# Optimization experiments

Hardware: AMD Instinct MI355X
Metric: run time of the kernel (lower is better)

## Reference

```python
import jax, jax.numpy as jnp
import numpy as np

NX, NA, T = 128, 64, 1024
MU = 1.0          # self.mu at entry to backward_pass
EPS = 1e-8        # singular-value clamp (self.eps)


def setup_inputs() -> dict:
    key = jax.random.key(0)
    ks = jax.random.split(key, 7)
    sx = 0.3 / np.sqrt(NX)  # keep dynamics spectral norm < 1 so recursion is stable
    fx = jax.random.normal(ks[0], (T, NX, NX), dtype=jnp.float32) * sx
    fa = jax.random.normal(ks[1], (T, NX, NA), dtype=jnp.float32) * sx
    lx = jax.random.normal(ks[2], (T, NX), dtype=jnp.float32)
    la = jax.random.normal(ks[3], (T, NA), dtype=jnp.float32)
    A = jax.random.normal(ks[4], (T, NX, NX), dtype=jnp.float32) * 0.1
    lxx = 0.5 * (A + A.transpose(0, 2, 1)) + jnp.eye(NX, dtype=jnp.float32)
    B = jax.random.normal(ks[5], (T, NA, NA), dtype=jnp.float32) * 0.1
    laa = 0.5 * (B + B.transpose(0, 2, 1)) + jnp.eye(NA, dtype=jnp.float32)
    lax = jax.random.normal(ks[6], (T, NA, NX), dtype=jnp.float32) * 0.1
    return dict(fx=fx, fa=fa, lx=lx, la=la, lxx=lxx, laa=laa, lax=lax)


def reference(fx, fa, lx, la, lxx, laa, lax):
    """iLQR backward Riccati recursion (ILQR.backward_pass + ILQR.q).
    Returns gains [T, na, 1+nx]: column 0 is k (feedforward), columns 1: are K
    (feedback), ordered by ascending time t=0..T-1."""
    I = jnp.eye(NX, dtype=fx.dtype)

    def step(carry, inp):
        Vx, Vxx = carry
        fx_t, fa_t, lx_t, la_t, lxx_t, laa_t, lax_t = inp
        # Q-function expansion (ILQR.q)
        Qx = lx_t + fx_t.T @ Vx
        Qa = la_t + fa_t.T @ Vx
        Qxx = lxx_t + fx_t.T @ Vxx @ fx_t
        Vreg = Vxx + MU * I
        Qax = lax_t + fa_t.T @ Vreg @ fx_t
        Qaa = laa_t + fa_t.T @ Vreg @ fa_t
        # SVD-based regularized inverse (S[S<eps] = eps)
        U, S, Vh = jnp.linalg.svd(Qaa)
        S = jnp.maximum(S, EPS)
        Vm = Vh.T
        Qaa_inv = (Vm * (1.0 / S)) @ U.T   # V diag(1/S) U^T
        Qaa_r = (U * S) @ Vm.T             # U diag(S) V^T (reconstructed Qaa)
        k = -Qaa_inv @ Qa
        K = -Qaa_inv @ Qax
        # value-function recursion
        Vx_n = Qx + K.T @ (Qaa_r @ k) + K.T @ Qa + Qax.T @ k
        Vxx_n = Qxx + K.T @ Qaa_r @ K + K.T @ Qax + Qax.T @ K
        Vxx_n = 0.5 * (Vxx_n + Vxx_n.T)
        return (Vx_n, Vxx_n), jnp.concatenate([k[:, None], K], axis=1)

    init = (lx[-1], lxx[-1])  # terminal Vx, Vxx
    (_, _), gains = jax.lax.scan(step, init, (fx, fa, lx, la, lxx, laa, lax), reverse=True)
    return gains
```

## Files before the change

kernel.cpp:

```cpp
#include <hip/hip_runtime.h>
#include <math.h>

#define TSTEPS 1024
#define NXD 128
#define NAD 64
#define NBLK 64
#define LSTR 67
#define QSTR 65
#define KSTR 68
#define GAINW 129

__device__ __forceinline__ float rdl(float v, int l) {
  return __int_as_float(__builtin_amdgcn_readlane(__float_as_int(v), l));
}
__device__ __forceinline__ double rdl(double v, int l) {
  unsigned long long b = (unsigned long long)__double_as_longlong(v);
  int lo = __builtin_amdgcn_readlane((int)(b & 0xffffffffULL), l);
  int hi = __builtin_amdgcn_readlane((int)(b >> 32), l);
  unsigned long long r = (((unsigned long long)(unsigned)hi) << 32) | (unsigned)lo;
  return __longlong_as_double((long long)r);
}

__device__ __forceinline__ float factor32(const float* __restrict__ QaaS, int lane,
                                          float* __restrict__ Lsh) {
  float a[64];
#pragma unroll
  for (int k = 0; k < 64; ++k) a[k] = QaaS[lane * QSTR + k];
  float mmax = 0.f;
#pragma unroll
  for (int j = 0; j < 63; ++j) {
    float d = rdl(a[j], j);
    d = (d == 0.f) ? 1e-30f : d;
    float rdv = 1.0f / d;
    float m = a[j] * rdv;
    m = (lane > j) ? m : 0.f;
    mmax = fmaxf(mmax, fabsf(m));
#pragma unroll
    for (int k = j + 1; k < 64; ++k) {
      float u = rdl(a[j], k);
      a[k] = fmaf(-m, u, a[k]);
    }
    if (lane > j) a[j] = m;
  }
#pragma unroll
  for (int k = 0; k < 64; ++k) Lsh[lane * LSTR + k] = a[k];
#pragma unroll
  for (int s = 1; s < 64; s <<= 1) mmax = fmaxf(mmax, __shfl_xor(mmax, s));
  return mmax;
}

__device__ __forceinline__ void factor64(const float* __restrict__ QaaS, int lane,
                                         double* __restrict__ Lsh) {
  double a[64];
#pragma unroll
  for (int k = 0; k < 64; ++k) a[k] = (double)QaaS[lane * QSTR + k];
#pragma unroll
  for (int j = 0; j < 63; ++j) {
    double d = rdl(a[j], j);
    d = (d == 0.0) ? 1e-300 : d;
    double rdv = 1.0 / d;
    double m = a[j] * rdv;
    m = (lane > j) ? m : 0.0;
#pragma unroll
    for (int k = j + 1; k < 64; ++k) {
      double u = rdl(a[j], k);
      a[k] = fma(-m, u, a[k]);
    }
    if (lane > j) a[j] = m;
  }
#pragma unroll
  for (int k = 0; k < 64; ++k) Lsh[lane * LSTR + k] = a[k];
}

template <typename T>
__device__ __forceinline__ void trisolveN(const T* __restrict__ Lsh, int lane,
                                          const float bv[9], float g[9]) {
  T x[9];
#pragma unroll
  for (int r = 0; r < 9; ++r) x[r] = (T)bv[r];
  for (int j = 0; j < 63; ++j) {
    T lij = Lsh[lane * LSTR + j];
#pragma unroll
    for (int r = 0; r < 9; ++r) {
      T xj = rdl(x[r], j);
      if (lane > j) x[r] = x[r] - lij * xj;
    }
  }
  T d = Lsh[lane * LSTR + lane];
  if (d == (T)0) d = (T)1e-30;
#pragma unroll
  for (int r = 0; r < 9; ++r) x[r] = x[r] / d;
  for (int j = 63; j > 0; --j) {
    T lji = Lsh[j * LSTR + lane];
#pragma unroll
    for (int r = 0; r < 9; ++r) {
      T xj = rdl(x[r], j);
      if (lane < j) x[r] = x[r] - lji * xj;
    }
  }
#pragma unroll
  for (int r = 0; r < 9; ++r) g[r] = -(float)x[r];
}

__device__ __forceinline__ void matvec128_lds(const float* __restrict__ VxxS, float fcl, float fch,
                                              int lane, float& w0, float& w1) {
  w0 = 0.f; w1 = 0.f;
  const float* vrow = VxxS + 2 * lane;
#pragma unroll 8
  for (int c = 0; c < 64; ++c) {
    float s = rdl(fcl, c);
    float2 v = *(const float2*)(vrow + c * NXD);
    w0 = fmaf(v.x, s, w0); w1 = fmaf(v.y, s, w1);
  }
#pragma unroll 8
  for (int c = 0; c < 64; ++c) {
    float s = rdl(fch, c);
    float2 v = *(const float2*)(vrow + (64 + c) * NXD);
    w0 = fmaf(v.x, s, w0); w1 = fmaf(v.y, s, w1);
  }
}

__global__ __launch_bounds__(256, 1) void k_init(const float* __restrict__ lxx,
                                                 const float* __restrict__ lx,
                                                 float* __restrict__ wsf) {
  float* Vxx = wsf;
  float* Vx  = wsf + 16384;
  const float* src = lxx + (size_t)(TSTEPS - 1) * NXD * NXD;
  int idx = blockIdx.x * 256 + threadIdx.x;
  Vxx[idx] = src[idx];
  if (blockIdx.x == 0 && threadIdx.x < NXD) Vx[threadIdx.x] = lx[(size_t)(TSTEPS - 1) * NXD + threadIdx.x];
}

__global__ __launch_bounds__(256, 1) void k_assemble(
    const float* __restrict__ fx, const float* __restrict__ fa,
    const float* __restrict__ lx, const float* __restrict__ la,
    const float* __restrict__ lxx, const float* __restrict__ laa,
    const float* __restrict__ lax, float* __restrict__ wsf, int t) {

  __shared__ float VxxS[NXD * NXD];

  const int b = blockIdx.x;
  const int tid = threadIdx.x;
  const int wave = tid >> 6;
  const int lane = tid & 63;

  float* Vxx  = wsf;
  float* Vx   = Vxx + 16384;
  float* QxxC = Vx + 128;
  float* QaxT = QxxC + 16384;
  float* QaaC = QaxT + 8192;
  float* Qx   = QaaC + 4096;
  float* Qa   = Qx + 128;

  const float* fxt  = fx  + (size_t)t * NXD * NXD;
  const float* fat  = fa  + (size_t)t * NXD * NAD;
  const float* lxt  = lx  + (size_t)t * NXD;
  const float* lat  = la  + (size_t)t * NAD;
  const float* lxxt = lxx + (size_t)t * NXD * NXD;
  const float* laat = laa + (size_t)t * NAD * NAD;
  const float* laxt = lax + (size_t)t * NAD * NXD;

  {
    const float4* Vg4 = (const float4*)Vxx;
    float4* Vs4 = (float4*)VxxS;
#pragma unroll
    for (int q = 0; q < 16; ++q) Vs4[tid + 256 * q] = Vg4[tid + 256 * q];
  }
  __syncthreads();

  if (wave <= 1) {
    const int j = 2 * b + wave;
    float pf0 = fxt[lane * NXD + j];
    float pf1 = fxt[(64 + lane) * NXD + j];
    float w0, w1;
    matvec128_lds(VxxS, pf0, pf1, lane, w0, w1);
    float q0 = lxxt[(size_t)(2 * lane) * NXD + j];
    float q1 = lxxt[(size_t)(2 * lane + 1) * NXD + j];
    float qa = laxt[lane * NXD + j];
#pragma unroll 4
    for (int r2 = 0; r2 < 32; ++r2) {
      float s0 = rdl(w0, r2), s1 = rdl(w1, r2);
      float t0 = s0 + rdl(pf0, 2 * r2);
      float t1 = s1 + rdl(pf0, 2 * r2 + 1);
      float2 f0 = *(const float2*)(fxt + (size_t)(2 * r2) * NXD + 2 * lane);
      float2 f1 = *(const float2*)(fxt + (size_t)(2 * r2 + 1) * NXD + 2 * lane);
      float g0 = fat[(2 * r2) * NAD + lane];
      float g1 = fat[(2 * r2 + 1) * NAD + lane];
      q0 = fmaf(f0.x, s0, q0); q1 = fmaf(f0.y, s0, q1);
      q0 = fmaf(f1.x, s1, q0); q1 = fmaf(f1.y, s1, q1);
      qa = fmaf(g0, t0, qa);   qa = fmaf(g1, t1, qa);
    }
#pragma unroll 4
    for (int r2 = 32; r2 < 64; ++r2) {
      float s0 = rdl(w0, r2), s1 = rdl(w1, r2);
      float t0 = s0 + rdl(pf1, 2 * r2 - 64);
      float t1 = s1 + rdl(pf1, 2 * r2 + 1 - 64);
      float2 f0 = *(const float2*)(fxt + (size_t)(2 * r2) * NXD + 2 * lane);
      float2 f1 = *(const float2*)(fxt + (size_t)(2 * r2 + 1) * NXD + 2 * lane);
      float g0 = fat[(2 * r2) * NAD + lane];
      float g1 = fat[(2 * r2 + 1) * NAD + lane];
      q0 = fmaf(f0.x, s0, q0); q1 = fmaf(f0.y, s0, q1);
      q0 = fmaf(f1.x, s1, q0); q1 = fmaf(f1.y, s1, q1);
      qa = fmaf(g0, t0, qa);   qa = fmaf(g1, t1, qa);
    }
    QxxC[(size_t)j * NXD + 2 * lane] = q0;
    QxxC[(size_t)j * NXD + 2 * lane + 1] = q1;
    QaxT[j * NAD + lane] = qa;
  } else if (wave == 2) {
    const int j = b;
    float pf0 = fat[lane * NAD + j];
    float pf1 = fat[(64 + lane) * NAD + j];
    float w0, w1;
    matvec128_lds(VxxS, pf0, pf1, lane, w0, w1);
    float qa = laat[lane * NAD + j];
#pragma unroll 4
    for (int r2 = 0; r2 < 32; ++r2) {
      float t0 = rdl(w0, r2) + rdl(pf0, 2 * r2);
      float t1 = rdl(w1, r2) + rdl(pf0, 2 * r2 + 1);
      float g0 = fat[(2 * r2) * NAD + lane];
      float g1 = fat[(2 * r2 + 1) * NAD + lane];
      qa = fmaf(g0, t0, qa); qa = fmaf(g1, t1, qa);
    }
#pragma unroll 4
    for (int r2 = 32; r2 < 64; ++r2) {
      float t0 = rdl(w0, r2) + rdl(pf1, 2 * r2 - 64);
      float t1 = rdl(w1, r2) + rdl(pf1, 2 * r2 + 1 - 64);
      float g0 = fat[(2 * r2) * NAD + lane];
      float g1 = fat[(2 * r2 + 1) * NAD + lane];
      qa = fmaf(g0, t0, qa); qa = fmaf(g1, t1, qa);
    }
    QaaC[j * NAD + lane] = qa;
  } else {
    float pv0 = Vx[lane], pv1 = Vx[64 + lane];
#pragma unroll
    for (int q = 0; q < 3; ++q) {
      int rr = 3 * b + q;
      float f0, f1;
      if (rr < NXD) { f0 = fxt[lane * NXD + rr]; f1 = fxt[(64 + lane) * NXD + rr]; }
      else { int aa = rr - NXD; f0 = fat[lane * NAD + aa]; f1 = fat[(64 + lane) * NAD + aa]; }
      float p = f0 * pv0 + f1 * pv1;
#pragma unroll
      for (int s = 1; s < 64; s <<= 1) p += __shfl_xor(p, s);
      if (lane == 0) {
        if (rr < NXD) Qx[rr] = lxt[rr] + p;
        else          Qa[rr - NXD] = lat[rr - NXD] + p;
      }
    }
  }
}

__global__ __launch_bounds__(256, 1) void k_solve_update(
    float* __restrict__ out, float* __restrict__ wsf, int t) {

  __shared__ float  QaaS[NAD * QSTR];
  __shared__ float  LfS[NAD * LSTR];
  __shared__ double LdS[NAD * LSTR];
  __shared__ float  KS[33 * KSTR];
  __shared__ float  QaxS[32 * KSTR];
  __shared__ int flag64;

  const int b = blockIdx.x;
  const int tid = threadIdx.x;
  const int wave = tid >> 6;
  const int lane = tid & 63;
  const int ti = b >> 3, tj = b & 7;

  float* Vxx  = wsf;
  float* Vx   = Vxx + 16384;
  float* QxxC = Vx + 128;
  float* QaxT = QxxC + 16384;
  float* QaaC = QaxT + 8192;
  float* Qx   = QaaC + 4096;
  float* Qa   = Qx + 128;

#pragma unroll
  for (int q = 0; q < 16; ++q) {
    int idx = tid + 256 * q;
    QaaS[(idx >> 6) * QSTR + (idx & 63)] = QaaC[idx];
  }
  float bv[9];
#pragma unroll
  for (int r = 0; r < 9; ++r) {
    int slot = wave + 4 * r;
    float v = 0.f;
    if (slot < 33) {
      int m = (slot < 16) ? (1 + 16 * tj + slot)
            : (slot < 32) ? (1 + 16 * ti + (slot - 16)) : 0;
      v = (slot == 32) ? Qa[lane] : QaxT[(size_t)(m - 1) * NAD + lane];
      if (slot < 32) QaxS[slot * KSTR + lane] = v;
    }
    bv[r] = v;
  }
  __syncthreads();
  if (wave == 0) {
    float mmax = factor32(QaaS, lane, LfS);
    if (lane == 0) flag64 = !(mmax <= 64.0f);
  }
  __syncthreads();
  if (flag64 && wave == 0) factor64(QaaS, lane, LdS);
  __syncthreads();
  {
    float g[9];
    if (!flag64) trisolveN<float >(LfS, lane, bv, g);
    else         trisolveN<double>(LdS, lane, bv, g);
#pragma unroll
    for (int r = 0; r < 9; ++r) {
      int slot = wave + 4 * r;
      if (slot < 33) {
        KS[slot * KSTR + lane] = g[r];
        int m = (slot < 16) ? (1 + 16 * tj + slot)
              : (slot < 32) ? (1 + 16 * ti + (slot - 16)) : 0;
        bool writer = (slot < 16) ? (ti == 0) : (slot == 32 && b == 0);
        if (writer) out[(size_t)t * NAD * GAINW + (size_t)lane * GAINW + m] = g[r];
      }
    }
  }
  __syncthreads();

  {
    int il = tid >> 4, jl = tid & 15;
    int i = ti * 16 + il, j = tj * 16 + jl;
    float d1 = 0.f, d2 = 0.f;
    const float* qi = QaxS + (16 + il) * KSTR;
    const float* qj = QaxS + jl * KSTR;
    const float* kj = KS + jl * KSTR;
    const float* ki = KS + (16 + il) * KSTR;
#pragma unroll 4
    for (int a4 = 0; a4 < 16; ++a4) {
      float4 A = *(const float4*)(qi + 4 * a4);
      float4 B = *(const float4*)(kj + 4 * a4);
      float4 C = *(const float4*)(qj + 4 * a4);
      float4 D = *(const float4*)(ki + 4 * a4);
      d1 = fmaf(A.x, B.x, d1); d1 = fmaf(A.y, B.y, d1);
      d1 = fmaf(A.z, B.z, d1); d1 = fmaf(A.w, B.w, d1);
      d2 = fmaf(C.x, D.x, d2); d2 = fmaf(C.y, D.y, d2);
      d2 = fmaf(C.z, D.z, d2); d2 = fmaf(C.w, D.w, d2);
    }
    float v = 0.5f * (QxxC[(size_t)j * NXD + i] + QxxC[(size_t)i * NXD + j])
            + 0.5f * (d1 + d2);
    Vxx[(size_t)i * NXD + j] = v;

    if (ti == tj && jl == 0) {
      float acc = 0.f;
      const float* k0 = KS + 32 * KSTR;
#pragma unroll 4
      for (int a4 = 0; a4 < 16; ++a4) {
        float4 A = *(const float4*)(qi + 4 * a4);
        float4 B = *(const float4*)(k0 + 4 * a4);
        acc = fmaf(A.x, B.x, acc); acc = fmaf(A.y, B.y, acc);
        acc = fmaf(A.z, B.z, acc); acc = fmaf(A.w, B.w, acc);
      }
      Vx[i] = Qx[i] + acc;
    }
  }
}

extern "C" void kernel_launch(void* const* d_in, const int* in_sizes, int n_in,
                              void* d_out, int out_size, void* d_ws, size_t ws_size,
                              hipStream_t stream) {
  const float* fx  = (const float*)d_in[0];
  const float* fa  = (const float*)d_in[1];
  const float* lx  = (const float*)d_in[2];
  const float* la  = (const float*)d_in[3];
  const float* lxx = (const float*)d_in[4];
  const float* laa = (const float*)d_in[5];
  const float* lax = (const float*)d_in[6];
  float* out = (float*)d_out;
  float* wsf = (float*)d_ws;

  hipLaunchKernelGGL(k_init, dim3(NBLK), dim3(256), 0, stream, lxx, lx, wsf);
  for (int t = TSTEPS - 1; t >= 0; --t) {
    hipLaunchKernelGGL(k_assemble, dim3(NBLK), dim3(256), 0, stream,
                       fx, fa, lx, la, lxx, laa, lax, wsf, t);
    hipLaunchKernelGGL(k_solve_update, dim3(NBLK), dim3(256), 0, stream, out, wsf, t);
  }
}
```

Baseline: 52.13 ms.

## Fuse per-step launches into one persistent cooperative kernel with XCD-local grid barrier

Replaces the 2048 per-timestep kernel launches with a single cooperative persistent kernel. The kernel elects 32 blocks of 512 threads that share one XCD and synchronises them with an L2-scoped atomic grid barrier between the assemble and solve/update phases. Work is repartitioned across fewer, larger blocks (32x16 Vxx tiles, 7 RHS per wave). The goal is to remove launch overhead and keep the barrier traffic inside one XCD's L2, at the cost of using fewer CUs and depending on a spin barrier with an abort timeout.

```diff
diff --git a/kernel.cpp b/kernel.cpp
--- a/kernel.cpp
+++ b/kernel.cpp
@@ -4,11 +4,13 @@
 #define TSTEPS 1024
 #define NXD 128
 #define NAD 64
-#define NBLK 64
+#define NW 32
+#define TPB 512
 #define LSTR 67
 #define QSTR 65
 #define KSTR 68
 #define GAINW 129
+#define HWREG_XCC_ID 63508
 
 __device__ __forceinline__ float rdl(float v, int l) {
   return __int_as_float(__builtin_amdgcn_readlane(__float_as_int(v), l));
@@ -19,6 +21,47 @@
   int hi = __builtin_amdgcn_readlane((int)(b >> 32), l);
   unsigned long long r = (((unsigned long long)(unsigned)hi) << 32) | (unsigned)lo;
   return __longlong_as_double((long long)r);
+}
+
+__device__ __forceinline__ unsigned atomAddL2(unsigned* p, unsigned v) {
+  unsigned old;
+  asm volatile("global_atomic_add %0, %1, %2, off sc0\n\ts_waitcnt vmcnt(0)"
+               : "=v"(old) : "v"(p), "v"(v) : "memory");
+  return old;
+}
+__device__ __forceinline__ void stU32L2(unsigned* p, unsigned v) {
+  asm volatile("global_store_dword %0, %1, off sc0\n\ts_waitcnt vmcnt(0)"
+               :: "v"(p), "v"(v) : "memory");
+}
+
+__device__ __forceinline__ bool gbarL2(unsigned* arrive, unsigned* epoch, unsigned* abortW,
+                                       unsigned e, volatile int* sAbort) {
+  asm volatile("s_waitcnt vmcnt(0)" ::: "memory");
+  __syncthreads();
+  if (threadIdx.x == 0) {
+    *sAbort = 0;
+    unsigned prev = atomAddL2(arrive, 1u);
+    if (prev == e * NW - 1u) {
+      atomAddL2(epoch, 1u);
+    } else {
+      unsigned it = 0;
+      for (;;) {
+        if (atomAddL2(epoch, 0u) >= e) break;
+        if ((++it & 255u) == 0u) {
+          if (atomAddL2(abortW, 0u) != 0u) { *sAbort = 1; break; }
+          if (it > 4000000u) {
+            stU32L2(abortW, 1u);
+            stU32L2(epoch, 0x7FFFFFFFu);
+            *sAbort = 1; break;
+          }
+        }
+        __builtin_amdgcn_s_sleep(1);
+      }
+    }
+  }
+  __syncthreads();
+  asm volatile("buffer_inv sc0" ::: "memory");
+  return *sAbort == 0;
 }
 
 __device__ __forceinline__ float factor32(const float* __restrict__ QaaS, int lane,
@@ -72,16 +115,16 @@
   for (int k = 0; k < 64; ++k) Lsh[lane * LSTR + k] = a[k];
 }
 
-template <typename T>
+template <typename T, int N>
 __device__ __forceinline__ void trisolveN(const T* __restrict__ Lsh, int lane,
-                                          const float bv[9], float g[9]) {
-  T x[9];
-#pragma unroll
-  for (int r = 0; r < 9; ++r) x[r] = (T)bv[r];
+                                          const float bv[N], float g[N]) {
+  T x[N];
+#pragma unroll
+  for (int r = 0; r < N; ++r) x[r] = (T)bv[r];
   for (int j = 0; j < 63; ++j) {
     T lij = Lsh[lane * LSTR + j];
 #pragma unroll
-    for (int r = 0; r < 9; ++r) {
+    for (int r = 0; r < N; ++r) {
       T xj = rdl(x[r], j);
       if (lane > j) x[r] = x[r] - lij * xj;
     }
@@ -89,17 +132,17 @@
   T d = Lsh[lane * LSTR + lane];
   if (d == (T)0) d = (T)1e-30;
 #pragma unroll
-  for (int r = 0; r < 9; ++r) x[r] = x[r] / d;
+  for (int r = 0; r < N; ++r) x[r] = x[r] / d;
   for (int j = 63; j > 0; --j) {
     T lji = Lsh[j * LSTR + lane];
 #pragma unroll
-    for (int r = 0; r < 9; ++r) {
+    for (int r = 0; r < N; ++r) {
       T xj = rdl(x[r], j);
       if (lane < j) x[r] = x[r] - lji * xj;
     }
   }
 #pragma unroll
-  for (int r = 0; r < 9; ++r) g[r] = -(float)x[r];
+  for (int r = 0; r < N; ++r) g[r] = -(float)x[r];
 }
 
 __device__ __forceinline__ void matvec128_lds(const float* __restrict__ VxxS, float fcl, float fch,
@@ -120,29 +163,65 @@
   }
 }
 
-__global__ __launch_bounds__(256, 1) void k_init(const float* __restrict__ lxx,
-                                                 const float* __restrict__ lx,
-                                                 float* __restrict__ wsf) {
-  float* Vxx = wsf;
-  float* Vx  = wsf + 16384;
-  const float* src = lxx + (size_t)(TSTEPS - 1) * NXD * NXD;
-  int idx = blockIdx.x * 256 + threadIdx.x;
-  Vxx[idx] = src[idx];
-  if (blockIdx.x == 0 && threadIdx.x < NXD) Vx[threadIdx.x] = lx[(size_t)(TSTEPS - 1) * NXD + threadIdx.x];
-}
-
-__global__ __launch_bounds__(256, 1) void k_assemble(
+__global__ void init_bar_kernel(unsigned* bar) {
+  int i = threadIdx.x;
+#pragma unroll
+  for (int q = 0; q < 4; ++q) {
+    int idx = i + 256 * q;
+    unsigned v = (idx == 384) ? 0xFFFFFFFFu : 0u;
+    __hip_atomic_store(bar + idx, v, __ATOMIC_RELAXED, __HIP_MEMORY_SCOPE_AGENT);
+  }
+}
+
+__global__ __launch_bounds__(TPB, 1) void ilqr_main(
     const float* __restrict__ fx, const float* __restrict__ fa,
     const float* __restrict__ lx, const float* __restrict__ la,
     const float* __restrict__ lxx, const float* __restrict__ laa,
-    const float* __restrict__ lax, float* __restrict__ wsf, int t) {
-
-  __shared__ float VxxS[NXD * NXD];
-
-  const int b = blockIdx.x;
+    const float* __restrict__ lax, float* __restrict__ out,
+    float* __restrict__ wsf, unsigned* __restrict__ bar) {
+
+  __shared__ float SM[25088];
+  float*  VxxS = SM;
+  float*  QaaS = SM;
+  float*  LfS  = SM + 4160;
+  float*  KS   = SM + 8448;
+  float*  QaxS = SM + 11780;
+  double* LdS  = (double*)(SM + 16384);
+  __shared__ int flag64;
+  __shared__ unsigned sRank;
+  __shared__ int sAbort;
+
   const int tid = threadIdx.x;
-  const int wave = tid >> 6;
+
+  unsigned* arrive = bar + 0;
+  unsigned* epoch  = bar + 128;
+  unsigned* cnt    = bar + 256;
+  unsigned* leader = bar + 384;
+  unsigned* abortW = bar + 512;
+
+  if (tid == 0) {
+    unsigned xcd = ((unsigned)__builtin_amdgcn_s_getreg(HWREG_XCC_ID)) & 7u;
+    unsigned slot = __hip_atomic_fetch_add(cnt + xcd, 1u, __ATOMIC_RELAXED, __HIP_MEMORY_SCOPE_AGENT);
+    if (slot == NW - 1u) {
+      unsigned exp = 0xFFFFFFFFu;
+      __hip_atomic_compare_exchange_strong(leader, &exp, xcd, __ATOMIC_RELAXED,
+                                           __ATOMIC_RELAXED, __HIP_MEMORY_SCOPE_AGENT);
+    }
+    unsigned L; unsigned it = 0;
+    while ((L = __hip_atomic_load(leader, __ATOMIC_RELAXED, __HIP_MEMORY_SCOPE_AGENT)) == 0xFFFFFFFFu) {
+      __builtin_amdgcn_s_sleep(8);
+      if (++it > 2000000u) break;
+    }
+    sRank = (L != 0xFFFFFFFFu && L == xcd && slot < NW) ? slot : 0xFFFFFFFFu;
+  }
+  __syncthreads();
+  const unsigned rank = sRank;
+  if (rank >= NW) return;
+  const int b = (int)rank;
+
+  const int w = tid >> 6;
   const int lane = tid & 63;
+  const int ti = b >> 3, tj = b & 7;
 
   float* Vxx  = wsf;
   float* Vx   = Vxx + 16384;
@@ -152,206 +231,198 @@
   float* Qx   = QaaC + 4096;
   float* Qa   = Qx + 128;
 
-  const float* fxt  = fx  + (size_t)t * NXD * NXD;
-  const float* fat  = fa  + (size_t)t * NXD * NAD;
-  const float* lxt  = lx  + (size_t)t * NXD;
-  const float* lat  = la  + (size_t)t * NAD;
-  const float* lxxt = lxx + (size_t)t * NXD * NXD;
-  const float* laat = laa + (size_t)t * NAD * NAD;
-  const float* laxt = lax + (size_t)t * NAD * NXD;
+  unsigned ep = 0;
 
   {
-    const float4* Vg4 = (const float4*)Vxx;
-    float4* Vs4 = (float4*)VxxS;
-#pragma unroll
-    for (int q = 0; q < 16; ++q) Vs4[tid + 256 * q] = Vg4[tid + 256 * q];
-  }
-  __syncthreads();
-
-  if (wave <= 1) {
-    const int j = 2 * b + wave;
-    float pf0 = fxt[lane * NXD + j];
-    float pf1 = fxt[(64 + lane) * NXD + j];
-    float w0, w1;
-    matvec128_lds(VxxS, pf0, pf1, lane, w0, w1);
-    float q0 = lxxt[(size_t)(2 * lane) * NXD + j];
-    float q1 = lxxt[(size_t)(2 * lane + 1) * NXD + j];
-    float qa = laxt[lane * NXD + j];
-#pragma unroll 4
-    for (int r2 = 0; r2 < 32; ++r2) {
-      float s0 = rdl(w0, r2), s1 = rdl(w1, r2);
-      float t0 = s0 + rdl(pf0, 2 * r2);
-      float t1 = s1 + rdl(pf0, 2 * r2 + 1);
-      float2 f0 = *(const float2*)(fxt + (size_t)(2 * r2) * NXD + 2 * lane);
-      float2 f1 = *(const float2*)(fxt + (size_t)(2 * r2 + 1) * NXD + 2 * lane);
-      float g0 = fat[(2 * r2) * NAD + lane];
-      float g1 = fat[(2 * r2 + 1) * NAD + lane];
-      q0 = fmaf(f0.x, s0, q0); q1 = fmaf(f0.y, s0, q1);
-      q0 = fmaf(f1.x, s1, q0); q1 = fmaf(f1.y, s1, q1);
-      qa = fmaf(g0, t0, qa);   qa = fmaf(g1, t1, qa);
-    }
-#pragma unroll 4
-    for (int r2 = 32; r2 < 64; ++r2) {
-      float s0 = rdl(w0, r2), s1 = rdl(w1, r2);
-      float t0 = s0 + rdl(pf1, 2 * r2 - 64);
-      float t1 = s1 + rdl(pf1, 2 * r2 + 1 - 64);
-      float2 f0 = *(const float2*)(fxt + (size_t)(2 * r2) * NXD + 2 * lane);
-      float2 f1 = *(const float2*)(fxt + (size_t)(2 * r2 + 1) * NXD + 2 * lane);
-      float g0 = fat[(2 * r2) * NAD + lane];
-      float g1 = fat[(2 * r2 + 1) * NAD + lane];
-      q0 = fmaf(f0.x, s0, q0); q1 = fmaf(f0.y, s0, q1);
-      q0 = fmaf(f1.x, s1, q0); q1 = fmaf(f1.y, s1, q1);
-      qa = fmaf(g0, t0, qa);   qa = fmaf(g1, t1, qa);
-    }
-    QxxC[(size_t)j * NXD + 2 * lane] = q0;
-    QxxC[(size_t)j * NXD + 2 * lane + 1] = q1;
-    QaxT[j * NAD + lane] = qa;
-  } else if (wave == 2) {
-    const int j = b;
-    float pf0 = fat[lane * NAD + j];
-    float pf1 = fat[(64 + lane) * NAD + j];
-    float w0, w1;
-    matvec128_lds(VxxS, pf0, pf1, lane, w0, w1);
-    float qa = laat[lane * NAD + j];
-#pragma unroll 4
-    for (int r2 = 0; r2 < 32; ++r2) {
-      float t0 = rdl(w0, r2) + rdl(pf0, 2 * r2);
-      float t1 = rdl(w1, r2) + rdl(pf0, 2 * r2 + 1);
-      float g0 = fat[(2 * r2) * NAD + lane];
-      float g1 = fat[(2 * r2 + 1) * NAD + lane];
-      qa = fmaf(g0, t0, qa); qa = fmaf(g1, t1, qa);
-    }
-#pragma unroll 4
-    for (int r2 = 32; r2 < 64; ++r2) {
-      float t0 = rdl(w0, r2) + rdl(pf1, 2 * r2 - 64);
-      float t1 = rdl(w1, r2) + rdl(pf1, 2 * r2 + 1 - 64);
-      float g0 = fat[(2 * r2) * NAD + lane];
-      float g1 = fat[(2 * r2 + 1) * NAD + lane];
-      qa = fmaf(g0, t0, qa); qa = fmaf(g1, t1, qa);
-    }
-    QaaC[j * NAD + lane] = qa;
-  } else {
-    float pv0 = Vx[lane], pv1 = Vx[64 + lane];
-#pragma unroll
-    for (int q = 0; q < 3; ++q) {
-      int rr = 3 * b + q;
-      float f0, f1;
-      if (rr < NXD) { f0 = fxt[lane * NXD + rr]; f1 = fxt[(64 + lane) * NXD + rr]; }
-      else { int aa = rr - NXD; f0 = fat[lane * NAD + aa]; f1 = fat[(64 + lane) * NAD + aa]; }
-      float p = f0 * pv0 + f1 * pv1;
-#pragma unroll
-      for (int s = 1; s < 64; s <<= 1) p += __shfl_xor(p, s);
-      if (lane == 0) {
-        if (rr < NXD) Qx[rr] = lxt[rr] + p;
-        else          Qa[rr - NXD] = lat[rr - NXD] + p;
-      }
-    }
-  }
-}
-
-__global__ __launch_bounds__(256, 1) void k_solve_update(
-    float* __restrict__ out, float* __restrict__ wsf, int t) {
-
-  __shared__ float  QaaS[NAD * QSTR];
-  __shared__ float  LfS[NAD * LSTR];
-  __shared__ double LdS[NAD * LSTR];
-  __shared__ float  KS[33 * KSTR];
-  __shared__ float  QaxS[32 * KSTR];
-  __shared__ int flag64;
-
-  const int b = blockIdx.x;
-  const int tid = threadIdx.x;
-  const int wave = tid >> 6;
-  const int lane = tid & 63;
-  const int ti = b >> 3, tj = b & 7;
-
-  float* Vxx  = wsf;
-  float* Vx   = Vxx + 16384;
-  float* QxxC = Vx + 128;
-  float* QaxT = QxxC + 16384;
-  float* QaaC = QaxT + 8192;
-  float* Qx   = QaaC + 4096;
-  float* Qa   = Qx + 128;
-
-#pragma unroll
-  for (int q = 0; q < 16; ++q) {
-    int idx = tid + 256 * q;
-    QaaS[(idx >> 6) * QSTR + (idx & 63)] = QaaC[idx];
-  }
-  float bv[9];
-#pragma unroll
-  for (int r = 0; r < 9; ++r) {
-    int slot = wave + 4 * r;
-    float v = 0.f;
-    if (slot < 33) {
-      int m = (slot < 16) ? (1 + 16 * tj + slot)
-            : (slot < 32) ? (1 + 16 * ti + (slot - 16)) : 0;
-      v = (slot == 32) ? Qa[lane] : QaxT[(size_t)(m - 1) * NAD + lane];
-      if (slot < 32) QaxS[slot * KSTR + lane] = v;
-    }
-    bv[r] = v;
-  }
-  __syncthreads();
-  if (wave == 0) {
-    float mmax = factor32(QaaS, lane, LfS);
-    if (lane == 0) flag64 = !(mmax <= 64.0f);
-  }
-  __syncthreads();
-  if (flag64 && wave == 0) factor64(QaaS, lane, LdS);
-  __syncthreads();
-  {
-    float g[9];
-    if (!flag64) trisolveN<float >(LfS, lane, bv, g);
-    else         trisolveN<double>(LdS, lane, bv, g);
-#pragma unroll
-    for (int r = 0; r < 9; ++r) {
-      int slot = wave + 4 * r;
-      if (slot < 33) {
-        KS[slot * KSTR + lane] = g[r];
-        int m = (slot < 16) ? (1 + 16 * tj + slot)
-              : (slot < 32) ? (1 + 16 * ti + (slot - 16)) : 0;
-        bool writer = (slot < 16) ? (ti == 0) : (slot == 32 && b == 0);
-        if (writer) out[(size_t)t * NAD * GAINW + (size_t)lane * GAINW + m] = g[r];
-      }
-    }
-  }
-  __syncthreads();
-
-  {
-    int il = tid >> 4, jl = tid & 15;
-    int i = ti * 16 + il, j = tj * 16 + jl;
-    float d1 = 0.f, d2 = 0.f;
-    const float* qi = QaxS + (16 + il) * KSTR;
-    const float* qj = QaxS + jl * KSTR;
-    const float* kj = KS + jl * KSTR;
-    const float* ki = KS + (16 + il) * KSTR;
-#pragma unroll 4
-    for (int a4 = 0; a4 < 16; ++a4) {
-      float4 A = *(const float4*)(qi + 4 * a4);
-      float4 B = *(const float4*)(kj + 4 * a4);
-      float4 C = *(const float4*)(qj + 4 * a4);
-      float4 D = *(const float4*)(ki + 4 * a4);
-      d1 = fmaf(A.x, B.x, d1); d1 = fmaf(A.y, B.y, d1);
-      d1 = fmaf(A.z, B.z, d1); d1 = fmaf(A.w, B.w, d1);
-      d2 = fmaf(C.x, D.x, d2); d2 = fmaf(C.y, D.y, d2);
-      d2 = fmaf(C.z, D.z, d2); d2 = fmaf(C.w, D.w, d2);
-    }
-    float v = 0.5f * (QxxC[(size_t)j * NXD + i] + QxxC[(size_t)i * NXD + j])
-            + 0.5f * (d1 + d2);
-    Vxx[(size_t)i * NXD + j] = v;
-
-    if (ti == tj && jl == 0) {
-      float acc = 0.f;
-      const float* k0 = KS + 32 * KSTR;
+    const float* src = lxx + (size_t)(TSTEPS - 1) * NXD * NXD;
+    int idx = b * TPB + tid;
+    Vxx[idx] = src[idx];
+    if (b == 0 && tid < NXD) Vx[tid] = lx[(size_t)(TSTEPS - 1) * NXD + tid];
+  }
+  ++ep; if (!gbarL2(arrive, epoch, abortW, ep, &sAbort)) return;
+
+  for (int t = TSTEPS - 1; t >= 0; --t) {
+    const float* fxt  = fx  + (size_t)t * NXD * NXD;
+    const float* fat  = fa  + (size_t)t * NXD * NAD;
+    const float* lxt  = lx  + (size_t)t * NXD;
+    const float* lat  = la  + (size_t)t * NAD;
+    const float* lxxt = lxx + (size_t)t * NXD * NXD;
+    const float* laat = laa + (size_t)t * NAD * NAD;
+    const float* laxt = lax + (size_t)t * NAD * NXD;
+
+    {
+      const float4* Vg4 = (const float4*)Vxx;
+      float4* Vs4 = (float4*)VxxS;
+#pragma unroll
+      for (int q = 0; q < 8; ++q) Vs4[tid + TPB * q] = Vg4[tid + TPB * q];
+    }
+    __syncthreads();
+
+    if (w < 4) {
+      const int j = 4 * b + w;
+      float pf0 = fxt[lane * NXD + j];
+      float pf1 = fxt[(64 + lane) * NXD + j];
+      float w0, w1;
+      matvec128_lds(VxxS, pf0, pf1, lane, w0, w1);
+      float q0 = lxxt[(size_t)(2 * lane) * NXD + j];
+      float q1 = lxxt[(size_t)(2 * lane + 1) * NXD + j];
+      float qa = laxt[lane * NXD + j];
+#pragma unroll 4
+      for (int r2 = 0; r2 < 32; ++r2) {
+        float s0 = rdl(w0, r2), s1 = rdl(w1, r2);
+        float t0 = s0 + rdl(pf0, 2 * r2);
+        float t1 = s1 + rdl(pf0, 2 * r2 + 1);
+        float2 f0 = *(const float2*)(fxt + (size_t)(2 * r2) * NXD + 2 * lane);
+        float2 f1 = *(const float2*)(fxt + (size_t)(2 * r2 + 1) * NXD + 2 * lane);
+        float g0 = fat[(2 * r2) * NAD + lane];
+        float g1 = fat[(2 * r2 + 1) * NAD + lane];
+        q0 = fmaf(f0.x, s0, q0); q1 = fmaf(f0.y, s0, q1);
+        q0 = fmaf(f1.x, s1, q0); q1 = fmaf(f1.y, s1, q1);
+        qa = fmaf(g0, t0, qa);   qa = fmaf(g1, t1, qa);
+      }
+#pragma unroll 4
+      for (int r2 = 32; r2 < 64; ++r2) {
+        float s0 = rdl(w0, r2), s1 = rdl(w1, r2);
+        float t0 = s0 + rdl(pf1, 2 * r2 - 64);
+        float t1 = s1 + rdl(pf1, 2 * r2 + 1 - 64);
+        float2 f0 = *(const float2*)(fxt + (size_t)(2 * r2) * NXD + 2 * lane);
+        float2 f1 = *(const float2*)(fxt + (size_t)(2 * r2 + 1) * NXD + 2 * lane);
+        float g0 = fat[(2 * r2) * NAD + lane];
+        float g1 = fat[(2 * r2 + 1) * NAD + lane];
+        q0 = fmaf(f0.x, s0, q0); q1 = fmaf(f0.y, s0, q1);
+        q0 = fmaf(f1.x, s1, q0); q1 = fmaf(f1.y, s1, q1);
+        qa = fmaf(g0, t0, qa);   qa = fmaf(g1, t1, qa);
+      }
+      QxxC[(size_t)j * NXD + 2 * lane] = q0;
+      QxxC[(size_t)j * NXD + 2 * lane + 1] = q1;
+      QaxT[j * NAD + lane] = qa;
+    } else if (w < 6) {
+      const int j = 2 * b + (w - 4);
+      float pf0 = fat[lane * NAD + j];
+      float pf1 = fat[(64 + lane) * NAD + j];
+      float w0, w1;
+      matvec128_lds(VxxS, pf0, pf1, lane, w0, w1);
+      float qa = laat[lane * NAD + j];
+#pragma unroll 4
+      for (int r2 = 0; r2 < 32; ++r2) {
+        float t0 = rdl(w0, r2) + rdl(pf0, 2 * r2);
+        float t1 = rdl(w1, r2) + rdl(pf0, 2 * r2 + 1);
+        float g0 = fat[(2 * r2) * NAD + lane];
+        float g1 = fat[(2 * r2 + 1) * NAD + lane];
+        qa = fmaf(g0, t0, qa); qa = fmaf(g1, t1, qa);
+      }
+#pragma unroll 4
+      for (int r2 = 32; r2 < 64; ++r2) {
+        float t0 = rdl(w0, r2) + rdl(pf1, 2 * r2 - 64);
+        float t1 = rdl(w1, r2) + rdl(pf1, 2 * r2 + 1 - 64);
+        float g0 = fat[(2 * r2) * NAD + lane];
+        float g1 = fat[(2 * r2 + 1) * NAD + lane];
+        qa = fmaf(g0, t0, qa); qa = fmaf(g1, t1, qa);
+      }
+      QaaC[j * NAD + lane] = qa;
+    } else {
+      float pv0 = Vx[lane], pv1 = Vx[64 + lane];
+#pragma unroll
+      for (int q = 0; q < 3; ++q) {
+        int rr = 6 * b + 3 * (w - 6) + q;
+        float f0, f1;
+        if (rr < NXD) { f0 = fxt[lane * NXD + rr]; f1 = fxt[(64 + lane) * NXD + rr]; }
+        else { int aa = rr - NXD; f0 = fat[lane * NAD + aa]; f1 = fat[(64 + lane) * NAD + aa]; }
+        float p = f0 * pv0 + f1 * pv1;
+#pragma unroll
+        for (int s = 1; s < 64; s <<= 1) p += __shfl_xor(p, s);
+        if (lane == 0) {
+          if (rr < NXD) Qx[rr] = lxt[rr] + p;
+          else          Qa[rr - NXD] = lat[rr - NXD] + p;
+        }
+      }
+    }
+    ++ep; if (!gbarL2(arrive, epoch, abortW, ep, &sAbort)) return;
+
+#pragma unroll
+    for (int q = 0; q < 8; ++q) {
+      int idx = tid + TPB * q;
+      QaaS[(idx >> 6) * QSTR + (idx & 63)] = QaaC[idx];
+    }
+    float bv[7];
+#pragma unroll
+    for (int r = 0; r < 7; ++r) {
+      int s = w + 8 * r;
+      float v = 0.f;
+      if (s < 49) {
+        if (s == 48) v = Qa[lane];
+        else {
+          int c = (s < 16) ? (16 * tj + s) : (32 * ti + (s - 16));
+          v = QaxT[(size_t)c * NAD + lane];
+          QaxS[s * KSTR + lane] = v;
+        }
+      }
+      bv[r] = v;
+    }
+    __syncthreads();
+    if (w == 0) {
+      float mmax = factor32(QaaS, lane, LfS);
+      if (lane == 0) flag64 = !(mmax <= 64.0f);
+    }
+    __syncthreads();
+    if (flag64 && w == 0) factor64(QaaS, lane, LdS);
+    __syncthreads();
+    {
+      float g[7];
+      if (!flag64) trisolveN<float, 7>(LfS, lane, bv, g);
+      else         trisolveN<double, 7>(LdS, lane, bv, g);
+#pragma unroll
+      for (int r = 0; r < 7; ++r) {
+        int s = w + 8 * r;
+        if (s < 49) {
+          KS[s * KSTR + lane] = g[r];
+          bool writer = (s < 16 && ti == 0) || (s == 48 && b == 0);
+          if (writer) {
+            int m = (s < 16) ? (1 + 16 * tj + s) : 0;
+            out[(size_t)t * NAD * GAINW + (size_t)lane * GAINW + m] = g[r];
+          }
+        }
+      }
+    }
+    __syncthreads();
+
+    {
+      int il = tid >> 4, jl = tid & 15;
+      int i = 32 * ti + il, j = 16 * tj + jl;
+      float d1 = 0.f, d2 = 0.f;
+      const float* qi = QaxS + (16 + il) * KSTR;
+      const float* qj = QaxS + jl * KSTR;
+      const float* kj = KS + jl * KSTR;
+      const float* ki = KS + (16 + il) * KSTR;
 #pragma unroll 4
       for (int a4 = 0; a4 < 16; ++a4) {
         float4 A = *(const float4*)(qi + 4 * a4);
-        float4 B = *(const float4*)(k0 + 4 * a4);
-        acc = fmaf(A.x, B.x, acc); acc = fmaf(A.y, B.y, acc);
-        acc = fmaf(A.z, B.z, acc); acc = fmaf(A.w, B.w, acc);
-      }
-      Vx[i] = Qx[i] + acc;
-    }
+        float4 B = *(const float4*)(kj + 4 * a4);
+        float4 C = *(const float4*)(qj + 4 * a4);
+        float4 D = *(const float4*)(ki + 4 * a4);
+        d1 = fmaf(A.x, B.x, d1); d1 = fmaf(A.y, B.y, d1);
+        d1 = fmaf(A.z, B.z, d1); d1 = fmaf(A.w, B.w, d1);
+        d2 = fmaf(C.x, D.x, d2); d2 = fmaf(C.y, D.y, d2);
+        d2 = fmaf(C.z, D.z, d2); d2 = fmaf(C.w, D.w, d2);
+      }
+      float v = 0.5f * (QxxC[(size_t)j * NXD + i] + QxxC[(size_t)i * NXD + j])
+              + 0.5f * (d1 + d2);
+      Vxx[(size_t)i * NXD + j] = v;
+
+      if (tj == 0 && jl == 0) {
+        float acc = 0.f;
+        const float* k0 = KS + 48 * KSTR;
+#pragma unroll 4
+        for (int a4 = 0; a4 < 16; ++a4) {
+          float4 A = *(const float4*)(qi + 4 * a4);
+          float4 B = *(const float4*)(k0 + 4 * a4);
+          acc = fmaf(A.x, B.x, acc); acc = fmaf(A.y, B.y, acc);
+          acc = fmaf(A.z, B.z, acc); acc = fmaf(A.w, B.w, acc);
+        }
+        Vx[i] = Qx[i] + acc;
+      }
+    }
+    ++ep; if (!gbarL2(arrive, epoch, abortW, ep, &sAbort)) return;
   }
 }
 
@@ -366,12 +437,17 @@
   const float* laa = (const float*)d_in[5];
   const float* lax = (const float*)d_in[6];
   float* out = (float*)d_out;
-  float* wsf = (float*)d_ws;
-
-  hipLaunchKernelGGL(k_init, dim3(NBLK), dim3(256), 0, stream, lxx, lx, wsf);
-  for (int t = TSTEPS - 1; t >= 0; --t) {
-    hipLaunchKernelGGL(k_assemble, dim3(NBLK), dim3(256), 0, stream,
-                       fx, fa, lx, la, lxx, laa, lax, wsf, t);
-    hipLaunchKernelGGL(k_solve_update, dim3(NBLK), dim3(256), 0, stream, out, wsf, t);
-  }
-}
+
+  unsigned* bar = (unsigned*)d_ws;
+  float* wsf = (float*)((char*)d_ws + 8192);
+
+  hipLaunchKernelGGL(init_bar_kernel, dim3(1), dim3(256), 0, stream, bar);
+
+  void* args[10];
+  args[0] = (void*)&fx;  args[1] = (void*)&fa;  args[2] = (void*)&lx;
+  args[3] = (void*)&la;  args[4] = (void*)&lxx; args[5] = (void*)&laa;
+  args[6] = (void*)&lax; args[7] = (void*)&out; args[8] = (void*)&wsf;
+  args[9] = (void*)&bar;
+  hipLaunchCooperativeKernel((const void*)ilqr_main, dim3(256), dim3(TPB),
+                             args, 0, stream);
+}
```

Result: slower. 67.73 ms (+29.9%).
